# Kernel optimization log

Hardware: AMD Instinct MI355X
Metric: run time of the kernel (lower is better)

## Reference

```python
import jax, jax.numpy as jnp
import numpy as np

TOP_K = 2  # num_experts_per_tok


def setup_inputs() -> dict:
    key = jax.random.key(0)
    k1, k2, k3, k4, k5 = jax.random.split(key, 5)
    B, S, D, F, E = 2, 1024, 1024, 2048, 8
    return {
        "x": jax.random.normal(k1, (B, S, D), dtype=jnp.float32),
        "router_kernel_DE": jax.random.normal(k2, (D, E), dtype=jnp.float32) * 0.02,
        "kernel_gating_EDF": jax.random.normal(k3, (E, D, F), dtype=jnp.float32) * 0.02,
        "kernel_up_EDF": jax.random.normal(k4, (E, D, F), dtype=jnp.float32) * 0.02,
        "kernel_down_EFD": jax.random.normal(k5, (E, F, D), dtype=jnp.float32) * 0.02,
    }


def reference(x, router_kernel_DE, kernel_gating_EDF, kernel_up_EDF, kernel_down_EFD):
    E = router_kernel_DE.shape[-1]
    x = x.astype(jnp.float32)
    # --- Router ---
    logits_BSE = jnp.einsum('BSD,DE->BSE', x, router_kernel_DE)
    probs_BSE = jax.nn.softmax(logits_BSE.astype(jnp.float32), axis=-1)
    weights_BSK, indices_BSK = jax.lax.top_k(probs_BSE, TOP_K)
    norm_weights_BSK = jax.nn.softmax(weights_BSK, axis=-1)
    # scatter top-k weights into dense [B,S,E]
    one_hot_BSKE = jax.nn.one_hot(indices_BSK, num_classes=E, dtype=x.dtype)
    full_weights_BSE = jnp.sum(one_hot_BSKE * norm_weights_BSK[..., None], axis=2)
    # --- Dense-over-all-experts MoE forward ---
    gating_BSEF = jnp.einsum('BSD,EDF->BSEF', x, kernel_gating_EDF)
    act_BSEF = jax.nn.silu(gating_BSEF)
    up_BSEF = jnp.einsum('BSD,EDF->BSEF', x, kernel_up_EDF)
    fuse_BSEF = act_BSEF * up_BSEF
    down_BSED = jnp.einsum('BSEF,EFD->BSED', fuse_BSEF, kernel_down_EFD)
    out_BSD = jnp.einsum('BSED,BSE->BSD', down_BSED, full_weights_BSE)
    return out_BSD.astype(jnp.float32)
```

## Files before the change

kernel.cpp:

```cpp
#include <hip/hip_runtime.h>
#include <hip/hip_bf16.h>
#include <stdint.h>

#define T_TOK 2048
#define DIM 1024
#define FDIM 2048
#define NEXP 8
#define NSLOT 4096

typedef short bf16x8 __attribute__((ext_vector_type(8)));
typedef unsigned short u16x8 __attribute__((ext_vector_type(8)));
typedef float f32x4 __attribute__((ext_vector_type(4)));

__device__ __forceinline__ unsigned short f2bf(float f) {
  union { float f; unsigned int u; } v; v.f = f;
  unsigned int r = v.u + 0x7FFFu + ((v.u >> 16) & 1u);
  return (unsigned short)(r >> 16);
}

__device__ __forceinline__ float bf2f(unsigned short x) {
  union { unsigned int u; float f; } v; v.u = ((unsigned int)x) << 16;
  return v.f;
}

__device__ __forceinline__ void gld_lds16(const void* g, void* l) {
  __builtin_amdgcn_global_load_lds(
      (const __attribute__((address_space(1))) unsigned int*)g,
      (__attribute__((address_space(3))) unsigned int*)l, 16, 0, 0);
}

__global__ void router_kernel(const float* __restrict__ x, const float* __restrict__ rk,
                              int* __restrict__ counts, int* __restrict__ tok_e,
                              float* __restrict__ tok_w, unsigned short* __restrict__ xb) {
  int w = threadIdx.x >> 6, lane = threadIdx.x & 63;
  int t = blockIdx.x * 4 + w;
  float acc[NEXP];
#pragma unroll
  for (int e = 0; e < NEXP; ++e) acc[e] = 0.f;
  const float4* xr = (const float4*)(x + (size_t)t * DIM);
#pragma unroll
  for (int i = 0; i < 4; ++i) {
    float4 xv = xr[i * 64 + lane];
    uint2 pk;
    pk.x = ((unsigned)f2bf(xv.y) << 16) | f2bf(xv.x);
    pk.y = ((unsigned)f2bf(xv.w) << 16) | f2bf(xv.z);
    *(uint2*)(xb + (size_t)t * DIM + (i * 64 + lane) * 4) = pk;
    int d0 = (i * 64 + lane) * 4;
#pragma unroll
    for (int j = 0; j < 4; ++j) {
      const float4* rr = (const float4*)(rk + (size_t)(d0 + j) * NEXP);
      float4 r0 = rr[0], r1 = rr[1];
      float xs = (j == 0) ? xv.x : (j == 1) ? xv.y : (j == 2) ? xv.z : xv.w;
      acc[0] += xs * r0.x; acc[1] += xs * r0.y; acc[2] += xs * r0.z; acc[3] += xs * r0.w;
      acc[4] += xs * r1.x; acc[5] += xs * r1.y; acc[6] += xs * r1.z; acc[7] += xs * r1.w;
    }
  }
#pragma unroll
  for (int off = 32; off > 0; off >>= 1) {
#pragma unroll
    for (int e = 0; e < NEXP; ++e) acc[e] += __shfl_xor(acc[e], off, 64);
  }
  if (lane == 0) {
    float m = acc[0];
    for (int e = 1; e < NEXP; ++e) m = fmaxf(m, acc[e]);
    float p[NEXP], s = 0.f;
    for (int e = 0; e < NEXP; ++e) { p[e] = expf(acc[e] - m); s += p[e]; }
    float inv = 1.f / s;
    for (int e = 0; e < NEXP; ++e) p[e] *= inv;
    int i1 = 0;
    for (int e = 1; e < NEXP; ++e) if (p[e] > p[i1]) i1 = e;
    int i2 = (i1 == 0) ? 1 : 0;
    for (int e = 0; e < NEXP; ++e) if (e != i1 && p[e] > p[i2]) i2 = e;
    float e1 = expf(p[i1]), e2 = expf(p[i2]);
    float winv = 1.f / (e1 + e2);
    tok_e[t * 2] = i1; tok_e[t * 2 + 1] = i2;
    tok_w[t * 2] = e1 * winv; tok_w[t * 2 + 1] = e2 * winv;
    atomicAdd(&counts[i1], 1); atomicAdd(&counts[i2], 1);
  }
}

__global__ void assign_kernel(const int* __restrict__ tok_e, const float* __restrict__ tok_w,
                              const int* __restrict__ counts, int* __restrict__ cursor,
                              int* __restrict__ slot_token, float* __restrict__ slot_weight,
                              int* __restrict__ tok_slot) {
  int t = blockIdx.x * 256 + threadIdx.x;
  if (t >= T_TOK) return;
#pragma unroll
  for (int k = 0; k < 2; ++k) {
    int e = tok_e[t * 2 + k];
    int off = 0;
#pragma unroll
    for (int j = 0; j < NEXP; ++j) off += (j < e) ? counts[j] : 0;
    int pos = atomicAdd(&cursor[e], 1);
    int slot = off + pos;
    slot_token[slot] = t;
    slot_weight[slot] = tok_w[t * 2 + k];
    tok_slot[t * 2 + k] = slot;
  }
}

__global__ void transpose_all(const float* __restrict__ wg_f, const float* __restrict__ wu_f,
                              const float* __restrict__ wd_f, unsigned short* __restrict__ wgt,
                              unsigned short* __restrict__ wut, unsigned short* __restrict__ wdt) {
  __shared__ float lds[64][65];
  int bid = blockIdx.x, e = blockIdx.y;
  const float* in;
  unsigned short* out;
  int R, C, rb, cb;
  if (bid < 1024) {
    in = (bid < 512) ? wg_f : wu_f;
    out = (bid < 512) ? wgt : wut;
    int id = bid & 511;
    R = DIM; C = FDIM;
    cb = (id & 31) * 64; rb = (id >> 5) * 64;
  } else {
    in = wd_f; out = wdt;
    int id = bid - 1024;
    R = FDIM; C = DIM;
    cb = (id & 15) * 64; rb = (id >> 4) * 64;
  }
  size_t base = (size_t)e * (size_t)R * (size_t)C;
  int tid = threadIdx.x;
  int col4 = (tid & 15) * 4, row = tid >> 4;
#pragma unroll
  for (int it = 0; it < 4; ++it) {
    int r = row + it * 16;
    float4 v = *(const float4*)(in + base + (size_t)(rb + r) * C + cb + col4);
    lds[col4 + 0][r] = v.x; lds[col4 + 1][r] = v.y;
    lds[col4 + 2][r] = v.z; lds[col4 + 3][r] = v.w;
  }
  __syncthreads();
  int r4 = (tid & 15) * 4, c = tid >> 4;
#pragma unroll
  for (int it = 0; it < 4; ++it) {
    int cc = c + it * 16;
    uint2 v;
    v.x = ((unsigned)f2bf(lds[cc][r4 + 1]) << 16) | f2bf(lds[cc][r4]);
    v.y = ((unsigned)f2bf(lds[cc][r4 + 3]) << 16) | f2bf(lds[cc][r4 + 2]);
    *(uint2*)(out + base + (size_t)(cb + cc) * R + rb + r4) = v;
  }
}

__device__ __forceinline__ bool tile_decode(const int* counts, int ys, int& e, int& mt,
                                            int& off, int& cnt) {
  mt = ys; off = 0;
  for (e = 0; e < NEXP; ++e) {
    cnt = counts[e];
    int ntl = (cnt + 127) >> 7;
    if (mt < ntl) return true;
    mt -= ntl; off += cnt;
  }
  return false;
}

__global__ __launch_bounds__(256) void gemm_gateup(
    const unsigned short* __restrict__ xb, const unsigned short* __restrict__ wg,
    const unsigned short* __restrict__ wu, const int* __restrict__ counts,
    const int* __restrict__ slot_token, unsigned short* __restrict__ fuse) {
  int e, mt, off, cnt;
  if (!tile_decode(counts, blockIdx.y, e, mt, off, cnt)) return;
  int nt = blockIdx.x;
  __shared__ unsigned short Al[128 * 64];
  __shared__ unsigned short Bgl[64 * 64];
  __shared__ unsigned short Bul[64 * 64];
  int tid = threadIdx.x, w = tid >> 6, lane = tid & 63;
  int csrc = ((lane & 7) ^ (lane >> 3)) * 8;
  unsigned aoff[4];
  unsigned boff[2];
#pragma unroll
  for (int ii = 0; ii < 4; ++ii) {
    int r = (w * 4 + ii) * 8 + (lane >> 3);
    int row = mt * 128 + r;
    int tok = (row < cnt) ? slot_token[off + row] : 0;
    aoff[ii] = (unsigned)(tok * DIM + csrc);
  }
#pragma unroll
  for (int ii = 0; ii < 2; ++ii) {
    int r = (w * 2 + ii) * 8 + (lane >> 3);
    boff[ii] = (unsigned)((e * FDIM + nt * 64 + r) * DIM + csrc);
  }
  f32x4 accg[4][2] = {};
  f32x4 accu[4][2] = {};
  int wr = (w >> 1) * 64, wc = (w & 1) * 32;
  int swz = (lane & 7) << 3;
  int kof0 = ((lane >> 4) * 8) ^ swz;
  int kof1 = (32 + (lane >> 4) * 8) ^ swz;
  for (int k0 = 0; k0 < DIM; k0 += 64) {
#pragma unroll
    for (int ii = 0; ii < 4; ++ii)
      gld_lds16(xb + aoff[ii] + k0, &Al[(w * 4 + ii) * 512]);
#pragma unroll
    for (int ii = 0; ii < 2; ++ii) {
      gld_lds16(wg + boff[ii] + k0, &Bgl[(w * 2 + ii) * 512]);
      gld_lds16(wu + boff[ii] + k0, &Bul[(w * 2 + ii) * 512]);
    }
    __syncthreads();
#pragma unroll
    for (int kk = 0; kk < 2; ++kk) {
      int kof = kk ? kof1 : kof0;
      bf16x8 af[4], bg[2], bu[2];
#pragma unroll
      for (int q = 0; q < 4; ++q)
        af[q] = *(const bf16x8*)&Al[(wr + q * 16 + (lane & 15)) * 64 + kof];
#pragma unroll
      for (int q = 0; q < 2; ++q) {
        bg[q] = *(const bf16x8*)&Bgl[(wc + q * 16 + (lane & 15)) * 64 + kof];
        bu[q] = *(const bf16x8*)&Bul[(wc + q * 16 + (lane & 15)) * 64 + kof];
      }
#pragma unroll
      for (int m4 = 0; m4 < 4; ++m4) {
#pragma unroll
        for (int n4 = 0; n4 < 2; ++n4) {
          accg[m4][n4] = __builtin_amdgcn_mfma_f32_16x16x32_bf16(af[m4], bg[n4], accg[m4][n4], 0, 0, 0);
          accu[m4][n4] = __builtin_amdgcn_mfma_f32_16x16x32_bf16(af[m4], bu[n4], accu[m4][n4], 0, 0, 0);
        }
      }
    }
    __syncthreads();
  }
#pragma unroll
  for (int m4 = 0; m4 < 4; ++m4) {
#pragma unroll
    for (int n4 = 0; n4 < 2; ++n4) {
      f32x4 g = accg[m4][n4], u = accu[m4][n4];
#pragma unroll
      for (int j = 0; j < 4; ++j) {
        int r = wr + m4 * 16 + (lane >> 4) * 4 + j;
        int row = mt * 128 + r;
        if (row < cnt) {
          float gv = g[j];
          float val = gv / (1.f + expf(-gv)) * u[j];
          int f = nt * 64 + wc + n4 * 16 + (lane & 15);
          fuse[(size_t)(off + row) * FDIM + f] = f2bf(val);
        }
      }
    }
  }
}

__global__ __launch_bounds__(256) void gemm_down(
    const unsigned short* __restrict__ fuse, const unsigned short* __restrict__ wd,
    const int* __restrict__ counts, const float* __restrict__ slot_weight,
    unsigned short* __restrict__ part4) {
  int e, mt, off, cnt;
  if (!tile_decode(counts, blockIdx.y, e, mt, off, cnt)) return;
  int nt = blockIdx.x;
  int z = blockIdx.z;
  int kbase = z * (FDIM / 4);
  __shared__ unsigned short Al[128 * 64];
  __shared__ unsigned short Bl[128 * 64];
  int tid = threadIdx.x, w = tid >> 6, lane = tid & 63;
  int csrc = ((lane & 7) ^ (lane >> 3)) * 8;
  unsigned aoff[4];
  unsigned boff[4];
#pragma unroll
  for (int ii = 0; ii < 4; ++ii) {
    int r = (w * 4 + ii) * 8 + (lane >> 3);
    int row = mt * 128 + r;
    int grow = (row < cnt) ? (off + row) : off;
    aoff[ii] = (unsigned)(grow * FDIM + kbase + csrc);
    boff[ii] = (unsigned)((e * DIM + nt * 128 + r) * FDIM + kbase + csrc);
  }
  f32x4 acc[4][4] = {};
  int wr = (w >> 1) * 64, wc = (w & 1) * 64;
  int swz = (lane & 7) << 3;
  int kof0 = ((lane >> 4) * 8) ^ swz;
  int kof1 = (32 + (lane >> 4) * 8) ^ swz;
  for (int k0 = 0; k0 < FDIM / 4; k0 += 64) {
#pragma unroll
    for (int ii = 0; ii < 4; ++ii) {
      gld_lds16(fuse + aoff[ii] + k0, &Al[(w * 4 + ii) * 512]);
      gld_lds16(wd + boff[ii] + k0, &Bl[(w * 4 + ii) * 512]);
    }
    __syncthreads();
#pragma unroll
    for (int kk = 0; kk < 2; ++kk) {
      int kof = kk ? kof1 : kof0;
      bf16x8 af[4], bfr[4];
#pragma unroll
      for (int q = 0; q < 4; ++q) {
        af[q] = *(const bf16x8*)&Al[(wr + q * 16 + (lane & 15)) * 64 + kof];
        bfr[q] = *(const bf16x8*)&Bl[(wc + q * 16 + (lane & 15)) * 64 + kof];
      }
#pragma unroll
      for (int m4 = 0; m4 < 4; ++m4) {
#pragma unroll
        for (int n4 = 0; n4 < 4; ++n4) {
          acc[m4][n4] = __builtin_amdgcn_mfma_f32_16x16x32_bf16(af[m4], bfr[n4], acc[m4][n4], 0, 0, 0);
        }
      }
    }
    __syncthreads();
  }
#pragma unroll
  for (int m4 = 0; m4 < 4; ++m4) {
#pragma unroll
    for (int j = 0; j < 4; ++j) {
      int r = wr + m4 * 16 + (lane >> 4) * 4 + j;
      int row = mt * 128 + r;
      if (row < cnt) {
        float wgt = slot_weight[off + row];
#pragma unroll
        for (int n4 = 0; n4 < 4; ++n4) {
          int d = nt * 128 + wc + n4 * 16 + (lane & 15);
          part4[((size_t)z * NSLOT + off + row) * DIM + d] = f2bf(acc[m4][n4][j] * wgt);
        }
      }
    }
  }
}

__global__ void combine_kernel(const unsigned short* __restrict__ part4,
                               const int* __restrict__ tok_slot, float* __restrict__ out) {
  int i = blockIdx.x * 256 + threadIdx.x;
  int t = i >> 7;
  int c = i & 127;
  int s0 = tok_slot[t * 2], s1 = tok_slot[t * 2 + 1];
  const u16x8* base = (const u16x8*)part4;
  float o[8];
#pragma unroll
  for (int j = 0; j < 8; ++j) o[j] = 0.f;
#pragma unroll
  for (int z = 0; z < 4; ++z) {
    u16x8 a = base[((size_t)z * NSLOT + s0) * (DIM / 8) + c];
    u16x8 b = base[((size_t)z * NSLOT + s1) * (DIM / 8) + c];
#pragma unroll
    for (int j = 0; j < 8; ++j) o[j] += bf2f(a[j]) + bf2f(b[j]);
  }
  float4* dst = (float4*)(out + (size_t)t * DIM + c * 8);
  dst[0] = make_float4(o[0], o[1], o[2], o[3]);
  dst[1] = make_float4(o[4], o[5], o[6], o[7]);
}

extern "C" void kernel_launch(void* const* d_in, const int* in_sizes, int n_in,
                              void* d_out, int out_size, void* d_ws, size_t ws_size,
                              hipStream_t stream) {
  (void)in_sizes; (void)n_in; (void)out_size;
  const float* x    = (const float*)d_in[0];
  const float* rk   = (const float*)d_in[1];
  const float* wg_f = (const float*)d_in[2];
  const float* wu_f = (const float*)d_in[3];
  const float* wd_f = (const float*)d_in[4];
  float* out = (float*)d_out;

  char* ws = (char*)d_ws;
  size_t o_xb   = 0;
  size_t o_wg   = o_xb + (size_t)T_TOK * DIM * 2;
  size_t o_wu   = o_wg + (size_t)NEXP * FDIM * DIM * 2;
  size_t o_wd   = o_wu + (size_t)NEXP * FDIM * DIM * 2;
  size_t o_fuse = o_wd + (size_t)NEXP * DIM * FDIM * 2;
  size_t o_meta = o_fuse + (size_t)NSLOT * FDIM * 2;
  size_t o_counts = o_meta;
  size_t o_cursor = o_counts + 32;
  size_t o_tok_e  = o_cursor + 32;
  size_t o_tok_w  = o_tok_e + (size_t)T_TOK * 2 * 4;
  size_t o_tok_s  = o_tok_w + (size_t)T_TOK * 2 * 4;
  size_t o_st     = o_tok_s + (size_t)T_TOK * 2 * 4;
  size_t o_sw     = o_st + (size_t)NSLOT * 4;
  size_t need     = o_sw + (size_t)NSLOT * 4;
  if (ws_size < need) return;

  unsigned short* xb    = (unsigned short*)(ws + o_xb);
  unsigned short* wgt   = (unsigned short*)(ws + o_wg);
  unsigned short* wut   = (unsigned short*)(ws + o_wu);
  unsigned short* wdt   = (unsigned short*)(ws + o_wd);
  unsigned short* fuse  = (unsigned short*)(ws + o_fuse);
  unsigned short* part4 = (unsigned short*)(ws + o_wg);
  int* counts          = (int*)(ws + o_counts);
  int* cursor          = (int*)(ws + o_cursor);
  int* tok_e           = (int*)(ws + o_tok_e);
  float* tok_w         = (float*)(ws + o_tok_w);
  int* tok_slot        = (int*)(ws + o_tok_s);
  int* slot_token      = (int*)(ws + o_st);
  float* slot_weight   = (float*)(ws + o_sw);

  hipMemsetAsync(ws + o_counts, 0, 64, stream);
  router_kernel<<<T_TOK / 4, 256, 0, stream>>>(x, rk, counts, tok_e, tok_w, xb);
  assign_kernel<<<T_TOK / 256, 256, 0, stream>>>(tok_e, tok_w, counts, cursor,
                                                 slot_token, slot_weight, tok_slot);
  transpose_all<<<dim3(1536, NEXP), 256, 0, stream>>>(wg_f, wu_f, wd_f, wgt, wut, wdt);
  gemm_gateup<<<dim3(FDIM / 64, 40, 1), 256, 0, stream>>>(xb, wgt, wut, counts,
                                                          slot_token, fuse);
  gemm_down<<<dim3(DIM / 128, 40, 4), 256, 0, stream>>>(fuse, wdt, counts,
                                                        slot_weight, part4);
  combine_kernel<<<(T_TOK * DIM / 8) / 256, 256, 0, stream>>>(part4, tok_slot, out);
}
```

Baseline: 249.3 us.

## Fuse combine into down GEMM via atomic adds and widen transpose stores

The down-projection GEMM now scatters its weighted results straight into the fp32 output with atomicAdd, indexed by slot_token. This drops the bf16 split-K partial buffer, the tok_slot bookkeeping and the separate combine kernel, at the cost of a memset of the output and many fp32 atomics (8 contributions per output element). The weight transpose kernel also writes 16-byte vectors instead of 8-byte ones. Atomic accumulation makes the summation order nondeterministic.

```diff
diff --git a/kernel.cpp b/kernel.cpp
--- a/kernel.cpp
+++ b/kernel.cpp
@@ -9,18 +9,12 @@
 #define NSLOT 4096
 
 typedef short bf16x8 __attribute__((ext_vector_type(8)));
-typedef unsigned short u16x8 __attribute__((ext_vector_type(8)));
 typedef float f32x4 __attribute__((ext_vector_type(4)));
 
 __device__ __forceinline__ unsigned short f2bf(float f) {
   union { float f; unsigned int u; } v; v.f = f;
   unsigned int r = v.u + 0x7FFFu + ((v.u >> 16) & 1u);
   return (unsigned short)(r >> 16);
-}
-
-__device__ __forceinline__ float bf2f(unsigned short x) {
-  union { unsigned int u; float f; } v; v.u = ((unsigned int)x) << 16;
-  return v.f;
 }
 
 __device__ __forceinline__ void gld_lds16(const void* g, void* l) {
@@ -81,8 +75,7 @@
 
 __global__ void assign_kernel(const int* __restrict__ tok_e, const float* __restrict__ tok_w,
                               const int* __restrict__ counts, int* __restrict__ cursor,
-                              int* __restrict__ slot_token, float* __restrict__ slot_weight,
-                              int* __restrict__ tok_slot) {
+                              int* __restrict__ slot_token, float* __restrict__ slot_weight) {
   int t = blockIdx.x * 256 + threadIdx.x;
   if (t >= T_TOK) return;
 #pragma unroll
@@ -95,7 +88,6 @@
     int slot = off + pos;
     slot_token[slot] = t;
     slot_weight[slot] = tok_w[t * 2 + k];
-    tok_slot[t * 2 + k] = slot;
   }
 }
 
@@ -130,14 +122,16 @@
     lds[col4 + 2][r] = v.z; lds[col4 + 3][r] = v.w;
   }
   __syncthreads();
-  int r4 = (tid & 15) * 4, c = tid >> 4;
-#pragma unroll
-  for (int it = 0; it < 4; ++it) {
-    int cc = c + it * 16;
-    uint2 v;
-    v.x = ((unsigned)f2bf(lds[cc][r4 + 1]) << 16) | f2bf(lds[cc][r4]);
-    v.y = ((unsigned)f2bf(lds[cc][r4 + 3]) << 16) | f2bf(lds[cc][r4 + 2]);
-    *(uint2*)(out + base + (size_t)(cb + cc) * R + rb + r4) = v;
+  int r8 = (tid & 7) * 8, c = tid >> 3;
+#pragma unroll
+  for (int it = 0; it < 2; ++it) {
+    int cc = c + it * 32;
+    uint4 v;
+    v.x = ((unsigned)f2bf(lds[cc][r8 + 1]) << 16) | f2bf(lds[cc][r8 + 0]);
+    v.y = ((unsigned)f2bf(lds[cc][r8 + 3]) << 16) | f2bf(lds[cc][r8 + 2]);
+    v.z = ((unsigned)f2bf(lds[cc][r8 + 5]) << 16) | f2bf(lds[cc][r8 + 4]);
+    v.w = ((unsigned)f2bf(lds[cc][r8 + 7]) << 16) | f2bf(lds[cc][r8 + 6]);
+    *(uint4*)(out + base + (size_t)(cb + cc) * R + rb + r8) = v;
   }
 }
 
@@ -241,7 +235,7 @@
 __global__ __launch_bounds__(256) void gemm_down(
     const unsigned short* __restrict__ fuse, const unsigned short* __restrict__ wd,
     const int* __restrict__ counts, const float* __restrict__ slot_weight,
-    unsigned short* __restrict__ part4) {
+    const int* __restrict__ slot_token, float* __restrict__ out) {
   int e, mt, off, cnt;
   if (!tile_decode(counts, blockIdx.y, e, mt, off, cnt)) return;
   int nt = blockIdx.x;
@@ -300,36 +294,15 @@
       int row = mt * 128 + r;
       if (row < cnt) {
         float wgt = slot_weight[off + row];
+        int tok = slot_token[off + row];
 #pragma unroll
         for (int n4 = 0; n4 < 4; ++n4) {
           int d = nt * 128 + wc + n4 * 16 + (lane & 15);
-          part4[((size_t)z * NSLOT + off + row) * DIM + d] = f2bf(acc[m4][n4][j] * wgt);
+          atomicAdd(out + (size_t)tok * DIM + d, acc[m4][n4][j] * wgt);
         }
       }
     }
   }
-}
-
-__global__ void combine_kernel(const unsigned short* __restrict__ part4,
-                               const int* __restrict__ tok_slot, float* __restrict__ out) {
-  int i = blockIdx.x * 256 + threadIdx.x;
-  int t = i >> 7;
-  int c = i & 127;
-  int s0 = tok_slot[t * 2], s1 = tok_slot[t * 2 + 1];
-  const u16x8* base = (const u16x8*)part4;
-  float o[8];
-#pragma unroll
-  for (int j = 0; j < 8; ++j) o[j] = 0.f;
-#pragma unroll
-  for (int z = 0; z < 4; ++z) {
-    u16x8 a = base[((size_t)z * NSLOT + s0) * (DIM / 8) + c];
-    u16x8 b = base[((size_t)z * NSLOT + s1) * (DIM / 8) + c];
-#pragma unroll
-    for (int j = 0; j < 8; ++j) o[j] += bf2f(a[j]) + bf2f(b[j]);
-  }
-  float4* dst = (float4*)(out + (size_t)t * DIM + c * 8);
-  dst[0] = make_float4(o[0], o[1], o[2], o[3]);
-  dst[1] = make_float4(o[4], o[5], o[6], o[7]);
 }
 
 extern "C" void kernel_launch(void* const* d_in, const int* in_sizes, int n_in,
@@ -354,8 +327,7 @@
   size_t o_cursor = o_counts + 32;
   size_t o_tok_e  = o_cursor + 32;
   size_t o_tok_w  = o_tok_e + (size_t)T_TOK * 2 * 4;
-  size_t o_tok_s  = o_tok_w + (size_t)T_TOK * 2 * 4;
-  size_t o_st     = o_tok_s + (size_t)T_TOK * 2 * 4;
+  size_t o_st     = o_tok_w + (size_t)T_TOK * 2 * 4;
   size_t o_sw     = o_st + (size_t)NSLOT * 4;
   size_t need     = o_sw + (size_t)NSLOT * 4;
   if (ws_size < need) return;
@@ -365,23 +337,21 @@
   unsigned short* wut   = (unsigned short*)(ws + o_wu);
   unsigned short* wdt   = (unsigned short*)(ws + o_wd);
   unsigned short* fuse  = (unsigned short*)(ws + o_fuse);
-  unsigned short* part4 = (unsigned short*)(ws + o_wg);
   int* counts          = (int*)(ws + o_counts);
   int* cursor          = (int*)(ws + o_cursor);
   int* tok_e           = (int*)(ws + o_tok_e);
   float* tok_w         = (float*)(ws + o_tok_w);
-  int* tok_slot        = (int*)(ws + o_tok_s);
   int* slot_token      = (int*)(ws + o_st);
   float* slot_weight   = (float*)(ws + o_sw);
 
   hipMemsetAsync(ws + o_counts, 0, 64, stream);
+  hipMemsetAsync(out, 0, (size_t)T_TOK * DIM * 4, stream);
   router_kernel<<<T_TOK / 4, 256, 0, stream>>>(x, rk, counts, tok_e, tok_w, xb);
   assign_kernel<<<T_TOK / 256, 256, 0, stream>>>(tok_e, tok_w, counts, cursor,
-                                                 slot_token, slot_weight, tok_slot);
+                                                 slot_token, slot_weight);
   transpose_all<<<dim3(1536, NEXP), 256, 0, stream>>>(wg_f, wu_f, wd_f, wgt, wut, wdt);
   gemm_gateup<<<dim3(FDIM / 64, 40, 1), 256, 0, stream>>>(xb, wgt, wut, counts,
                                                           slot_token, fuse);
   gemm_down<<<dim3(DIM / 128, 40, 4), 256, 0, stream>>>(fuse, wdt, counts,
-                                                        slot_weight, part4);
-  combine_kernel<<<(T_TOK * DIM / 8) / 256, 256, 0, stream>>>(part4, tok_slot, out);
-}
+                                                        slot_weight, slot_token, out);
+}
```

Result: slower. 278.1 us (+11.5%).

## Double-buffer LDS in gate/up GEMM and widen transpose stores to 16 bytes

Applied to the files above, without the earlier changes.

The gate/up expert GEMM now stages the next K-slice into a second LDS buffer while the current one feeds the MFMAs, with one barrier per iteration instead of two. The goal is to hide global-to-LDS load latency behind compute. The weight transpose/convert kernel also writes 8 bf16 values per thread as uint4 stores instead of 4 as uint2. LDS use for the GEMM doubles (to about 64KB), which may cut occupancy.

```diff
diff --git a/kernel.cpp b/kernel.cpp
--- a/kernel.cpp
+++ b/kernel.cpp
@@ -130,14 +130,16 @@
     lds[col4 + 2][r] = v.z; lds[col4 + 3][r] = v.w;
   }
   __syncthreads();
-  int r4 = (tid & 15) * 4, c = tid >> 4;
-#pragma unroll
-  for (int it = 0; it < 4; ++it) {
-    int cc = c + it * 16;
-    uint2 v;
-    v.x = ((unsigned)f2bf(lds[cc][r4 + 1]) << 16) | f2bf(lds[cc][r4]);
-    v.y = ((unsigned)f2bf(lds[cc][r4 + 3]) << 16) | f2bf(lds[cc][r4 + 2]);
-    *(uint2*)(out + base + (size_t)(cb + cc) * R + rb + r4) = v;
+  int r8 = (tid & 7) * 8, c = tid >> 3;
+#pragma unroll
+  for (int it = 0; it < 2; ++it) {
+    int cc = c + it * 32;
+    uint4 v;
+    v.x = ((unsigned)f2bf(lds[cc][r8 + 1]) << 16) | f2bf(lds[cc][r8 + 0]);
+    v.y = ((unsigned)f2bf(lds[cc][r8 + 3]) << 16) | f2bf(lds[cc][r8 + 2]);
+    v.z = ((unsigned)f2bf(lds[cc][r8 + 5]) << 16) | f2bf(lds[cc][r8 + 4]);
+    v.w = ((unsigned)f2bf(lds[cc][r8 + 7]) << 16) | f2bf(lds[cc][r8 + 6]);
+    *(uint4*)(out + base + (size_t)(cb + cc) * R + rb + r8) = v;
   }
 }
 
@@ -160,9 +162,9 @@
   int e, mt, off, cnt;
   if (!tile_decode(counts, blockIdx.y, e, mt, off, cnt)) return;
   int nt = blockIdx.x;
-  __shared__ unsigned short Al[128 * 64];
-  __shared__ unsigned short Bgl[64 * 64];
-  __shared__ unsigned short Bul[64 * 64];
+  __shared__ unsigned short Al[2][128 * 64];
+  __shared__ unsigned short Bgl[2][64 * 64];
+  __shared__ unsigned short Bul[2][64 * 64];
   int tid = threadIdx.x, w = tid >> 6, lane = tid & 63;
   int csrc = ((lane & 7) ^ (lane >> 3)) * 8;
   unsigned aoff[4];
@@ -185,27 +187,29 @@
   int swz = (lane & 7) << 3;
   int kof0 = ((lane >> 4) * 8) ^ swz;
   int kof1 = (32 + (lane >> 4) * 8) ^ swz;
-  for (int k0 = 0; k0 < DIM; k0 += 64) {
+
+  auto stage = [&](int buf, int k0) {
 #pragma unroll
     for (int ii = 0; ii < 4; ++ii)
-      gld_lds16(xb + aoff[ii] + k0, &Al[(w * 4 + ii) * 512]);
+      gld_lds16(xb + aoff[ii] + k0, &Al[buf][(w * 4 + ii) * 512]);
 #pragma unroll
     for (int ii = 0; ii < 2; ++ii) {
-      gld_lds16(wg + boff[ii] + k0, &Bgl[(w * 2 + ii) * 512]);
-      gld_lds16(wu + boff[ii] + k0, &Bul[(w * 2 + ii) * 512]);
-    }
-    __syncthreads();
+      gld_lds16(wg + boff[ii] + k0, &Bgl[buf][(w * 2 + ii) * 512]);
+      gld_lds16(wu + boff[ii] + k0, &Bul[buf][(w * 2 + ii) * 512]);
+    }
+  };
+  auto compute = [&](int buf) {
 #pragma unroll
     for (int kk = 0; kk < 2; ++kk) {
       int kof = kk ? kof1 : kof0;
       bf16x8 af[4], bg[2], bu[2];
 #pragma unroll
       for (int q = 0; q < 4; ++q)
-        af[q] = *(const bf16x8*)&Al[(wr + q * 16 + (lane & 15)) * 64 + kof];
+        af[q] = *(const bf16x8*)&Al[buf][(wr + q * 16 + (lane & 15)) * 64 + kof];
 #pragma unroll
       for (int q = 0; q < 2; ++q) {
-        bg[q] = *(const bf16x8*)&Bgl[(wc + q * 16 + (lane & 15)) * 64 + kof];
-        bu[q] = *(const bf16x8*)&Bul[(wc + q * 16 + (lane & 15)) * 64 + kof];
+        bg[q] = *(const bf16x8*)&Bgl[buf][(wc + q * 16 + (lane & 15)) * 64 + kof];
+        bu[q] = *(const bf16x8*)&Bul[buf][(wc + q * 16 + (lane & 15)) * 64 + kof];
       }
 #pragma unroll
       for (int m4 = 0; m4 < 4; ++m4) {
@@ -216,8 +220,22 @@
         }
       }
     }
-    __syncthreads();
-  }
+  };
+
+  stage(0, 0);
+  asm volatile("s_waitcnt vmcnt(0)" ::: "memory");
+  __builtin_amdgcn_s_barrier();
+  int cb = 0;
+  for (int k0 = 0; k0 < DIM; k0 += 64) {
+    if (k0 + 64 < DIM) stage(cb ^ 1, k0 + 64);
+    __builtin_amdgcn_sched_barrier(0);
+    compute(cb);
+    __builtin_amdgcn_sched_barrier(0);
+    asm volatile("s_waitcnt vmcnt(0)" ::: "memory");
+    __builtin_amdgcn_s_barrier();
+    cb ^= 1;
+  }
+
 #pragma unroll
   for (int m4 = 0; m4 < 4; ++m4) {
 #pragma unroll
```

New measurement: 244.8 us. Within noise of the previous version (-1.8%).
